# Kernel tuning notes

Measured on AMD Instinct MI355X. Metric: run time of the kernel, lower is better.

The kernel has to match this reference:

```python
import jax, jax.numpy as jnp
import numpy as np

B, H, W, C = 8, 64, 64, 512
G = 32  # num_groups
EPS = 1e-5


def group_norm(x, scale, bias):
    b, h, w, c = x.shape
    xg = x.reshape(b, h, w, G, c // G)
    mean = jnp.mean(xg, axis=(1, 2, 4), keepdims=True)
    var = jnp.var(xg, axis=(1, 2, 4), keepdims=True)
    xg = (xg - mean) / jnp.sqrt(var + EPS)
    x = xg.reshape(b, h, w, c)
    return x * scale + bias


def conv1x1(x, w, b):
    # NHWC 1x1 conv == channel matmul
    return jnp.einsum('bhwc,cd->bhwd', x, w) + b


def setup_inputs() -> dict:
    key = jax.random.key(0)
    ks = jax.random.split(key, 10)
    init = lambda k, shape: jax.random.normal(k, shape, dtype=jnp.float32) * (1.0 / np.sqrt(C))
    return {
        'x': jax.random.normal(ks[0], (B, H, W, C), dtype=jnp.float32),
        'gn_scale': jnp.ones((C,), dtype=jnp.float32),
        'gn_bias': jnp.zeros((C,), dtype=jnp.float32),
        'wq': init(ks[1], (C, C)), 'bq': jnp.zeros((C,), jnp.float32),
        'wk': init(ks[2], (C, C)), 'bk': jnp.zeros((C,), jnp.float32),
        'wv': init(ks[3], (C, C)), 'bv': jnp.zeros((C,), jnp.float32),
        'wo': init(ks[4], (C, C)), 'bo': jnp.zeros((C,), jnp.float32),
    }


def reference(x, gn_scale, gn_bias, wq, bq, wk, bk, wv, bv, wo, bo):
    h = group_norm(x, gn_scale, gn_bias)
    q = conv1x1(h, wq, bq)
    k = conv1x1(h, wk, bk)
    v = conv1x1(h, wv, bv)
    b, hh, ww, c = h.shape
    n = hh * ww
    q = q.reshape(b, n, c)
    k = k.reshape(b, n, c)
    v = v.reshape(b, n, c)
    scores = jnp.einsum('bqc,bkc->bqk', q, k) * (c ** -0.5)
    attn = jax.nn.softmax(scores, axis=-1)
    out = jnp.einsum('bqk,bkc->bqc', attn, v).reshape(b, hh, ww, c)
    out = conv1x1(out, wo, bo)
    return out + x
```

## Files before the change

kernel.cpp:

```cpp
#include <hip/hip_runtime.h>

typedef __bf16 bfx8 __attribute__((ext_vector_type(8)));
typedef __bf16 bfx4 __attribute__((ext_vector_type(4)));
typedef float  f32x4 __attribute__((ext_vector_type(4)));

#define MFMA16(a,b,c) __builtin_amdgcn_mfma_f32_16x16x32_bf16((a),(b),(c),0,0,0)

static constexpr int BATCH = 8;
static constexpr int NTOK  = 4096;
static constexpr int CH    = 512;
static constexpr float GN_EPS = 1e-5f;
static constexpr float ATT_SCALE = 0.044194173824159216f;

__device__ __forceinline__ void gload16(const void* g, void* l)
{
    __builtin_amdgcn_global_load_lds(
        (const __attribute__((address_space(1))) unsigned int*)g,
        (__attribute__((address_space(3))) unsigned int*)l, 16, 0, 0);
}

__global__ __launch_bounds__(256)
void prep_weights(const float* __restrict__ wq, const float* __restrict__ wk,
                  const float* __restrict__ wv, const float* __restrict__ wo,
                  const float* __restrict__ bq, const float* __restrict__ bk,
                  const float* __restrict__ bv,
                  __bf16* __restrict__ wqkvT, __bf16* __restrict__ woT,
                  float* __restrict__ bqkv)
{
    __shared__ __bf16 t[32][36];
    const int z  = blockIdx.z;
    const float* src = (z == 0) ? wq : (z == 1) ? wk : (z == 2) ? wv : wo;
    const int c0 = blockIdx.x * 32, n0 = blockIdx.y * 32;
    const int tid = threadIdx.x;
    const int r = tid >> 3, c4 = (tid & 7) * 4;

    f32x4 in = *(const f32x4*)&src[(size_t)(c0 + r) * 512 + n0 + c4];
    bfx4 tv;
#pragma unroll
    for (int i = 0; i < 4; ++i) tv[i] = (__bf16)in[i];
    *(bfx4*)&t[r][c4] = tv;
    __syncthreads();
    bfx4 o;
#pragma unroll
    for (int i = 0; i < 4; ++i) o[i] = t[c4 + i][r];
    if (z < 3)
        *(bfx4*)&wqkvT[((size_t)(z * 512 + n0 + r)) * 512 + c0 + c4] = o;
    else
        *(bfx4*)&woT[((size_t)(n0 + r)) * 512 + c0 + c4] = o;

    if (z < 3 && blockIdx.x == 0 && blockIdx.y == 0) {
        const float* bs = (z == 0) ? bq : (z == 1) ? bk : bv;
        bqkv[z * 512 + tid]       = bs[tid];
        bqkv[z * 512 + tid + 256] = bs[tid + 256];
    }
}

__global__ __launch_bounds__(256)
void gn_stats(const float* __restrict__ x, const float* __restrict__ gs,
              const float* __restrict__ gb,
              float* __restrict__ scA, float* __restrict__ biA)
{
    const int g = blockIdx.x, b = blockIdx.y;
    const int tid = threadIdx.x;
    const int half = tid & 1;
    const size_t base = (size_t)b * NTOK * CH + g * 16 + half * 8;

    float sum = 0.f, sumsq = 0.f;
    for (int i = tid; i < 2 * NTOK; i += 256) {
        const int s = i >> 1;
        f32x4 v0 = *(const f32x4*)&x[base + (size_t)s * CH];
        f32x4 v1 = *(const f32x4*)&x[base + (size_t)s * CH + 4];
#pragma unroll
        for (int j = 0; j < 4; ++j) {
            sum += v0[j] + v1[j];
            sumsq += v0[j] * v0[j] + v1[j] * v1[j];
        }
    }
#pragma unroll
    for (int o = 32; o; o >>= 1) { sum += __shfl_down(sum, o); sumsq += __shfl_down(sumsq, o); }
    __shared__ float red[8];
    __shared__ float stats[2];
    const int w = tid >> 6;
    if ((tid & 63) == 0) { red[w] = sum; red[4 + w] = sumsq; }
    __syncthreads();
    if (tid == 0) {
        float s1 = red[0] + red[1] + red[2] + red[3];
        float s2 = red[4] + red[5] + red[6] + red[7];
        float mean = s1 * (1.f / 65536.f);
        float var  = s2 * (1.f / 65536.f) - mean * mean;
        stats[0] = mean; stats[1] = rsqrtf(var + GN_EPS);
    }
    __syncthreads();
    if (tid < 16) {
        const int ch = g * 16 + tid;
        const float sc = gs[ch] * stats[1];
        scA[b * 512 + ch] = sc;
        biA[b * 512 + ch] = gb[ch] - stats[0] * sc;
    }
}

__global__ __launch_bounds__(256)
void gemm_qkv(const float* __restrict__ x, const float* __restrict__ scA,
              const float* __restrict__ biA, const __bf16* __restrict__ Bt,
              const float* __restrict__ bias,
              __bf16* __restrict__ qk, __bf16* __restrict__ vT)
{
    const int bm = blockIdx.x * 128, bn = blockIdx.y * 128;
    const int tid = threadIdx.x;
    const int w = tid >> 6, lane = tid & 63, quad = lane >> 4, l15 = lane & 15;
    const int wm = (w >> 1) * 64, wn = (w & 1) * 64;
    const int brow = bm >> 12;

    __shared__ __attribute__((aligned(16))) __bf16 smem_g[5120 + 2 * 128 * 32];
    __bf16 (*As)[40] = (__bf16(*)[40])smem_g;
    __bf16 (*Bs)[128][32] = (__bf16(*)[128][32])(smem_g + 5120);

    f32x4 acc[4][4];
#pragma unroll
    for (int i = 0; i < 4; ++i)
#pragma unroll
        for (int j = 0; j < 4; ++j) acc[i][j] = (f32x4){0.f, 0.f, 0.f, 0.f};

    const int sr = tid >> 2, scol = (tid & 3) * 8;
    const int brow_l = (lane >> 2);
    const int bcp    = lane & 3;

#pragma unroll
    for (int u = 0; u < 2; ++u) {
        const int row = w * 32 + u * 16 + brow_l;
        gload16(Bt + (size_t)(bn + row) * 512 + ((bcp ^ (row & 3)) * 8),
                &Bs[0][w * 32 + u * 16][0]);
    }
    f32x4 xa0 = *(const f32x4*)&x[(size_t)(bm + sr) * 512 + scol];
    f32x4 xa1 = *(const f32x4*)&x[(size_t)(bm + sr) * 512 + scol + 4];
    f32x4 xb0 = *(const f32x4*)&x[(size_t)(bm + sr + 64) * 512 + scol];
    f32x4 xb1 = *(const f32x4*)&x[(size_t)(bm + sr + 64) * 512 + scol + 4];

    for (int k0 = 0; k0 < 512; k0 += 32) {
        const int cur = (k0 >> 5) & 1;
        __syncthreads();
        {
            const float* scp = scA + brow * 512 + k0 + scol;
            const float* bip = biA + brow * 512 + k0 + scol;
            f32x4 s0v = *(const f32x4*)&scp[0], s1v = *(const f32x4*)&scp[4];
            f32x4 b0v = *(const f32x4*)&bip[0], b1v = *(const f32x4*)&bip[4];
            bfx8 ha, hb;
#pragma unroll
            for (int j = 0; j < 4; ++j) {
                ha[j]     = (__bf16)(xa0[j] * s0v[j] + b0v[j]);
                ha[4 + j] = (__bf16)(xa1[j] * s1v[j] + b1v[j]);
                hb[j]     = (__bf16)(xb0[j] * s0v[j] + b0v[j]);
                hb[4 + j] = (__bf16)(xb1[j] * s1v[j] + b1v[j]);
            }
            *(bfx8*)&As[sr][scol]      = ha;
            *(bfx8*)&As[sr + 64][scol] = hb;
        }
        if (k0 + 32 < 512) {
            const int k1 = k0 + 32;
#pragma unroll
            for (int u = 0; u < 2; ++u) {
                const int row = w * 32 + u * 16 + brow_l;
                gload16(Bt + (size_t)(bn + row) * 512 + k1 + ((bcp ^ (row & 3)) * 8),
                        &Bs[cur ^ 1][w * 32 + u * 16][0]);
            }
            xa0 = *(const f32x4*)&x[(size_t)(bm + sr) * 512 + k1 + scol];
            xa1 = *(const f32x4*)&x[(size_t)(bm + sr) * 512 + k1 + scol + 4];
            xb0 = *(const f32x4*)&x[(size_t)(bm + sr + 64) * 512 + k1 + scol];
            xb1 = *(const f32x4*)&x[(size_t)(bm + sr + 64) * 512 + k1 + scol + 4];
        }
        asm volatile("s_waitcnt lgkmcnt(0)\n\ts_barrier" ::: "memory");

        bfx8 af[4], bfr[4];
#pragma unroll
        for (int mi = 0; mi < 4; ++mi) af[mi] = *(const bfx8*)&As[wm + mi * 16 + l15][quad * 8];
#pragma unroll
        for (int ni = 0; ni < 4; ++ni) {
            const int row = wn + ni * 16 + l15;
            bfr[ni] = *(const bfx8*)&Bs[cur][row][(quad ^ (row & 3)) * 8];
        }
#pragma unroll
        for (int mi = 0; mi < 4; ++mi)
#pragma unroll
            for (int ni = 0; ni < 4; ++ni)
                acc[mi][ni] = MFMA16(af[mi], bfr[ni], acc[mi][ni]);
    }

    if (blockIdx.y < 8) {
        const float scale = (blockIdx.y < 4) ? ATT_SCALE : 1.0f;
#pragma unroll
        for (int ni = 0; ni < 4; ++ni) {
            const int col = bn + wn + ni * 16 + l15;
            const float bv = bias[col];
#pragma unroll
            for (int mi = 0; mi < 4; ++mi)
#pragma unroll
                for (int rr = 0; rr < 4; ++rr) {
                    const int row = bm + wm + mi * 16 + quad * 4 + rr;
                    qk[(size_t)row * 1024 + col] = (__bf16)((acc[mi][ni][rr] + bv) * scale);
                }
        }
    } else {
        const int vch0 = bn - 1024;
        const int tokbase = bm & 4095;
        __bf16* tb = smem_g;
        __syncthreads();
#pragma unroll
        for (int chunk = 0; chunk < 2; ++chunk) {
            if ((w & 1) == chunk) {
#pragma unroll
                for (int ni = 0; ni < 4; ++ni) {
                    const int chc = ni * 16 + l15;
                    const float bv = bias[bn + chunk * 64 + chc];
#pragma unroll
                    for (int mi = 0; mi < 4; ++mi)
#pragma unroll
                        for (int rr = 0; rr < 4; ++rr) {
                            const int tok = wm + mi * 16 + quad * 4 + rr;
                            tb[chc * 136 + tok] = (__bf16)(acc[mi][ni][rr] + bv);
                        }
                }
            }
            __syncthreads();
            {
                const int chn = tid >> 2, t0 = (tid & 3) * 32;
                const size_t gb0 =
                    ((size_t)(brow * 512 + vch0 + chunk * 64 + chn)) * 4096 + tokbase;
#pragma unroll
                for (int u = 0; u < 4; ++u)
                    *(bfx8*)&vT[gb0 + t0 + u * 8] = *(const bfx8*)&tb[chn * 136 + t0 + u * 8];
            }
            __syncthreads();
        }
    }
}

__global__ __launch_bounds__(512, 2)
void attn_fused(const __bf16* __restrict__ qk, const __bf16* __restrict__ vT,
                const __bf16* __restrict__ woT, const float* __restrict__ bo,
                const float* __restrict__ x, float* __restrict__ out)
{
    const int lin = blockIdx.x + (int)gridDim.x * blockIdx.y;
    const int swz = (lin & 7) * 32 + (lin >> 3);
    const int bb  = swz >> 5;
    const int q0  = (swz & 31) * 128;
    const int tid = threadIdx.x;
    const int w = tid >> 6, lane = tid & 63, quad = lane >> 4, l15 = lane & 15;

    __shared__ __attribute__((aligned(16))) unsigned char smem[141312];
    __bf16 (*Ks)[32][512]      = (__bf16(*)[32][512])smem;
    __bf16 (*Vs)[32][4][16][8] = (__bf16(*)[32][4][16][8])(smem + 65536);
    __bf16 (*Ph)[40]           = (__bf16(*)[40])(smem + 131072);
    __bf16 (*Obuf)[520]        = (__bf16(*)[520])smem;

    bfx8 qf[16];
    {
        const __bf16* qptr = qk + ((size_t)(bb * NTOK + q0 + w * 16 + l15)) * 1024;
#pragma unroll
        for (int kk = 0; kk < 16; ++kk)
            qf[kk] = *(const bfx8*)&qptr[kk * 32 + quad * 8];
    }

    f32x4 oacc[32];
#pragma unroll
    for (int i = 0; i < 32; ++i) oacc[i] = (f32x4){0.f, 0.f, 0.f, 0.f};
    float mcur = -1e30f, lcur = 0.f;

#pragma unroll
    for (int u = 0; u < 4; ++u) {
        const int r = w * 4 + u;
        gload16(qk + ((size_t)(bb * NTOK + r)) * 1024 + 512 + ((lane ^ (r & 7)) * 8),
                &Ks[0][r][0]);
    }
#pragma unroll
    for (int u = 0; u < 4; ++u) {
        const int g = w * 4 + u;
        gload16(vT + ((size_t)(bb * 512 + g * 16 + (lane & 15))) * 4096 + (lane >> 4) * 8,
                &Vs[0][g][0][0][0]);
    }

    const int NT = NTOK / 32;
    int buf = 0;
    for (int kt = 0; kt < NT; ++kt) {
        __syncthreads();

        if (kt + 1 < NT) {
            const int kv1 = (kt + 1) * 32;
            const int nb = buf ^ 1;
#pragma unroll
            for (int u = 0; u < 4; ++u) {
                const int r = w * 4 + u;
                gload16(qk + ((size_t)(bb * NTOK + kv1 + r)) * 1024 + 512 + ((lane ^ (r & 7)) * 8),
                        &Ks[nb][r][0]);
            }
#pragma unroll
            for (int u = 0; u < 4; ++u) {
                const int g = w * 4 + u;
                gload16(vT + ((size_t)(bb * 512 + g * 16 + (lane & 15))) * 4096 + kv1 + (lane >> 4) * 8,
                        &Vs[nb][g][0][0][0]);
            }
        }

        f32x4 s0 = (f32x4){0.f, 0.f, 0.f, 0.f}, s1 = (f32x4){0.f, 0.f, 0.f, 0.f};
        __builtin_amdgcn_s_setprio(1);
#pragma unroll
        for (int kk = 0; kk < 16; ++kk) {
            const int pc = (((kk * 4 + quad) ^ (l15 & 7)) * 8);
            bfx8 kb0 = *(const bfx8*)&Ks[buf][l15][pc];
            bfx8 kb1 = *(const bfx8*)&Ks[buf][16 + l15][pc];
            s0 = MFMA16(kb0, qf[kk], s0);
            s1 = MFMA16(kb1, qf[kk], s1);
        }
        __builtin_amdgcn_s_setprio(0);

        float mx = -1e30f;
#pragma unroll
        for (int i = 0; i < 4; ++i) mx = fmaxf(mx, fmaxf(s0[i], s1[i]));
        float ps = 0.f;
        bfx4 pl0, pl1;
#pragma unroll
        for (int i = 0; i < 4; ++i) { float p = __expf(s0[i] - mcur); ps += p; pl0[i] = (__bf16)p; }
#pragma unroll
        for (int i = 0; i < 4; ++i) { float p = __expf(s1[i] - mcur); ps += p; pl1[i] = (__bf16)p; }
        mx = fmaxf(mx, __shfl_xor(mx, 16));
        mx = fmaxf(mx, __shfl_xor(mx, 32));
        if (__builtin_expect(__any(mx > mcur + 8.f), 0)) {
            const float mnew = fmaxf(mcur, mx);
            const float al = __expf(mcur - mnew);
            lcur *= al;
            ps = 0.f;
#pragma unroll
            for (int i = 0; i < 4; ++i) { float p = __expf(s0[i] - mnew); ps += p; pl0[i] = (__bf16)p; }
#pragma unroll
            for (int i = 0; i < 4; ++i) { float p = __expf(s1[i] - mnew); ps += p; pl1[i] = (__bf16)p; }
            mcur = mnew;
#pragma unroll
            for (int ct = 0; ct < 32; ++ct)
#pragma unroll
                for (int r = 0; r < 4; ++r) oacc[ct][r] *= al;
        }

        *(bfx4*)&Ph[w * 16 + l15][quad * 4]      = pl0;
        *(bfx4*)&Ph[w * 16 + l15][16 + quad * 4] = pl1;

        asm volatile("s_waitcnt lgkmcnt(0)" ::: "memory");
        bfx8 pa = *(const bfx8*)&Ph[w * 16 + l15][quad * 8];

        __builtin_amdgcn_s_setprio(1);
#pragma unroll
        for (int ct = 0; ct < 32; ++ct) {
            bfx8 vb = *(const bfx8*)&Vs[buf][ct][quad][l15][0];
            oacc[ct] = MFMA16(vb, pa, oacc[ct]);
        }
        __builtin_amdgcn_s_setprio(0);

        ps += __shfl_xor(ps, 16);
        ps += __shfl_xor(ps, 32);
        lcur += ps;
        buf ^= 1;
    }

#pragma unroll
    for (int h = 0; h < 2; ++h) {
        __syncthreads();
        if ((w >> 2) == h) {
            const float linv = 1.f / lcur;
#pragma unroll
            for (int ct = 0; ct < 32; ++ct) {
                bfx4 ov;
#pragma unroll
                for (int r = 0; r < 4; ++r) ov[r] = (__bf16)(oacc[ct][r] * linv);
                *(bfx4*)&Obuf[(w & 3) * 16 + l15][ct * 16 + quad * 4] = ov;
            }
        }
        __syncthreads();

        const int rs  = (w & 3) * 16;
        const int nt0 = (w >> 2) * 16;
        bfx8 af2[16];
#pragma unroll
        for (int k0 = 0; k0 < 16; ++k0)
            af2[k0] = *(const bfx8*)&Obuf[rs + l15][k0 * 32 + quad * 8];
#pragma unroll 4
        for (int nt = 0; nt < 16; ++nt) {
            f32x4 a2 = (f32x4){0.f, 0.f, 0.f, 0.f};
#pragma unroll
            for (int k0 = 0; k0 < 16; ++k0) {
                bfx8 wb = *(const bfx8*)&woT[(size_t)((nt0 + nt) * 16 + l15) * 512 + k0 * 32 + quad * 8];
                a2 = MFMA16(af2[k0], wb, a2);
            }
            const int col = (nt0 + nt) * 16 + l15;
            const float bv = bo[col];
#pragma unroll
            for (int rr = 0; rr < 4; ++rr) {
                const size_t idx =
                    ((size_t)(bb * NTOK + q0 + h * 64 + rs + quad * 4 + rr)) * 512 + col;
                out[idx] = a2[rr] + bv + x[idx];
            }
        }
    }
}

extern "C" void kernel_launch(void* const* d_in, const int* in_sizes, int n_in,
                              void* d_out, int out_size, void* d_ws, size_t ws_size,
                              hipStream_t stream)
{
    const float* x  = (const float*)d_in[0];
    const float* gs = (const float*)d_in[1];
    const float* gb = (const float*)d_in[2];
    const float* wq = (const float*)d_in[3];
    const float* bq = (const float*)d_in[4];
    const float* wk = (const float*)d_in[5];
    const float* bk = (const float*)d_in[6];
    const float* wv = (const float*)d_in[7];
    const float* bv = (const float*)d_in[8];
    const float* wo = (const float*)d_in[9];
    const float* bo = (const float*)d_in[10];
    float* out = (float*)d_out;

    char* ws = (char*)d_ws;
    __bf16* qk    = (__bf16*)(ws);
    __bf16* vT    = (__bf16*)(ws + 67108864);
    __bf16* wqkvT = (__bf16*)(ws + 100663296);
    __bf16* woT   = (__bf16*)(ws + 102236160);
    float*  bqkv  = (float* )(ws + 102760448);
    float*  scA   = (float* )(ws + 102766592);
    float*  biA   = (float* )(ws + 102782976);

    prep_weights<<<dim3(16, 16, 4), 256, 0, stream>>>(wq, wk, wv, wo, bq, bk, bv,
                                                      wqkvT, woT, bqkv);
    gn_stats<<<dim3(32, BATCH), 256, 0, stream>>>(x, gs, gb, scA, biA);
    gemm_qkv<<<dim3(256, 12), 256, 0, stream>>>(x, scA, biA, wqkvT, bqkv, qk, vT);
    attn_fused<<<dim3(NTOK / 128, BATCH), 512, 0, stream>>>(qk, vT, woT, bo, x, out);
}
```

Measured before the change: 714.3 us.

## Store Q/K in FP8 and compute attention scores with FP8 MFMA

The QKV GEMM now writes Q and K as FP8 (e4m3) bytes instead of bf16, and the attention kernel computes QK^T with the fp8 16x16x32 MFMA, applying the softmax scale afterwards. This halves Q/K storage and the K tile traffic into LDS, shrinking shared memory per block. It also removes the last-iteration branch on prefetch by wrapping the tile index, and preloads the first four V fragments before the softmax to hide LDS latency. The trade-off is reduced precision in the attention scores, which may hurt accuracy.

```diff
diff --git a/kernel.cpp b/kernel.cpp
--- a/kernel.cpp
+++ b/kernel.cpp
@@ -5,6 +5,7 @@
 typedef float  f32x4 __attribute__((ext_vector_type(4)));
 
 #define MFMA16(a,b,c) __builtin_amdgcn_mfma_f32_16x16x32_bf16((a),(b),(c),0,0,0)
+#define MFMA16F8(a,b,c) __builtin_amdgcn_mfma_f32_16x16x32_fp8_fp8((a),(b),(c),0,0,0)
 
 static constexpr int BATCH = 8;
 static constexpr int NTOK  = 4096;
@@ -17,6 +18,11 @@
     __builtin_amdgcn_global_load_lds(
         (const __attribute__((address_space(1))) unsigned int*)g,
         (__attribute__((address_space(3))) unsigned int*)l, 16, 0, 0);
+}
+
+__device__ __forceinline__ int cvt2fp8(float a, float b)
+{
+    return __builtin_amdgcn_cvt_pk_fp8_f32(a, b, 0, false);
 }
 
 __global__ __launch_bounds__(256)
@@ -103,7 +109,7 @@
 void gemm_qkv(const float* __restrict__ x, const float* __restrict__ scA,
               const float* __restrict__ biA, const __bf16* __restrict__ Bt,
               const float* __restrict__ bias,
-              __bf16* __restrict__ qk, __bf16* __restrict__ vT)
+              unsigned char* __restrict__ qk8, __bf16* __restrict__ vT)
 {
     const int bm = blockIdx.x * 128, bn = blockIdx.y * 128;
     const int tid = threadIdx.x;
@@ -186,18 +192,20 @@
     }
 
     if (blockIdx.y < 8) {
-        const float scale = (blockIdx.y < 4) ? ATT_SCALE : 1.0f;
 #pragma unroll
         for (int ni = 0; ni < 4; ++ni) {
             const int col = bn + wn + ni * 16 + l15;
             const float bv = bias[col];
 #pragma unroll
-            for (int mi = 0; mi < 4; ++mi)
-#pragma unroll
-                for (int rr = 0; rr < 4; ++rr) {
-                    const int row = bm + wm + mi * 16 + quad * 4 + rr;
-                    qk[(size_t)row * 1024 + col] = (__bf16)((acc[mi][ni][rr] + bv) * scale);
-                }
+            for (int mi = 0; mi < 4; ++mi) {
+                const int row0 = bm + wm + mi * 16 + quad * 4;
+                const int p01 = cvt2fp8(acc[mi][ni][0] + bv, acc[mi][ni][1] + bv);
+                const int p23 = cvt2fp8(acc[mi][ni][2] + bv, acc[mi][ni][3] + bv);
+                qk8[(size_t)(row0 + 0) * 1024 + col] = (unsigned char)(p01 & 0xff);
+                qk8[(size_t)(row0 + 1) * 1024 + col] = (unsigned char)((p01 >> 8) & 0xff);
+                qk8[(size_t)(row0 + 2) * 1024 + col] = (unsigned char)(p23 & 0xff);
+                qk8[(size_t)(row0 + 3) * 1024 + col] = (unsigned char)((p23 >> 8) & 0xff);
+            }
         }
     } else {
         const int vch0 = bn - 1024;
@@ -235,7 +243,7 @@
 }
 
 __global__ __launch_bounds__(512, 2)
-void attn_fused(const __bf16* __restrict__ qk, const __bf16* __restrict__ vT,
+void attn_fused(const unsigned char* __restrict__ qk8, const __bf16* __restrict__ vT,
                 const __bf16* __restrict__ woT, const float* __restrict__ bo,
                 const float* __restrict__ x, float* __restrict__ out)
 {
@@ -246,18 +254,18 @@
     const int tid = threadIdx.x;
     const int w = tid >> 6, lane = tid & 63, quad = lane >> 4, l15 = lane & 15;
 
-    __shared__ __attribute__((aligned(16))) unsigned char smem[141312];
-    __bf16 (*Ks)[32][512]      = (__bf16(*)[32][512])smem;
-    __bf16 (*Vs)[32][4][16][8] = (__bf16(*)[32][4][16][8])(smem + 65536);
-    __bf16 (*Ph)[40]           = (__bf16(*)[40])(smem + 131072);
-    __bf16 (*Obuf)[520]        = (__bf16(*)[520])smem;
-
-    bfx8 qf[16];
+    __shared__ __attribute__((aligned(16))) unsigned char smem[108544];
+    unsigned char (*Ks8)[32][512] = (unsigned char(*)[32][512])smem;
+    __bf16 (*Vs)[32][4][16][8]    = (__bf16(*)[32][4][16][8])(smem + 32768);
+    __bf16 (*Ph)[40]              = (__bf16(*)[40])(smem + 98304);
+    __bf16 (*Obuf)[520]           = (__bf16(*)[520])smem;
+
+    long qf8[16];
     {
-        const __bf16* qptr = qk + ((size_t)(bb * NTOK + q0 + w * 16 + l15)) * 1024;
+        const unsigned char* qptr = qk8 + ((size_t)(bb * NTOK + q0 + w * 16 + l15)) * 1024;
 #pragma unroll
         for (int kk = 0; kk < 16; ++kk)
-            qf[kk] = *(const bfx8*)&qptr[kk * 32 + quad * 8];
+            qf8[kk] = *(const long*)(qptr + kk * 32 + quad * 8);
     }
 
     f32x4 oacc[32];
@@ -266,15 +274,16 @@
     float mcur = -1e30f, lcur = 0.f;
 
 #pragma unroll
-    for (int u = 0; u < 4; ++u) {
-        const int r = w * 4 + u;
-        gload16(qk + ((size_t)(bb * NTOK + r)) * 1024 + 512 + ((lane ^ (r & 7)) * 8),
-                &Ks[0][r][0]);
+    for (int u = 0; u < 2; ++u) {
+        const int r = w * 4 + u * 2 + (lane >> 5);
+        const int srcoff = ((2 * (lane & 31)) ^ ((r & 7) << 1)) * 8;
+        gload16(qk8 + ((size_t)(bb * NTOK + r)) * 1024 + 512 + srcoff,
+                &Ks8[0][w * 4 + u * 2][0]);
     }
 #pragma unroll
     for (int u = 0; u < 4; ++u) {
         const int g = w * 4 + u;
-        gload16(vT + ((size_t)(bb * 512 + g * 16 + (lane & 15))) * 4096 + (lane >> 4) * 8,
+        gload16(vT + ((size_t)(bb * 512 + g * 16 + l15)) * 4096 + quad * 8,
                 &Vs[0][g][0][0][0]);
     }
 
@@ -283,19 +292,20 @@
     for (int kt = 0; kt < NT; ++kt) {
         __syncthreads();
 
-        if (kt + 1 < NT) {
-            const int kv1 = (kt + 1) * 32;
+        {
+            const int kv1 = ((kt + 1) & (NT - 1)) * 32;
             const int nb = buf ^ 1;
 #pragma unroll
-            for (int u = 0; u < 4; ++u) {
-                const int r = w * 4 + u;
-                gload16(qk + ((size_t)(bb * NTOK + kv1 + r)) * 1024 + 512 + ((lane ^ (r & 7)) * 8),
-                        &Ks[nb][r][0]);
+            for (int u = 0; u < 2; ++u) {
+                const int r = w * 4 + u * 2 + (lane >> 5);
+                const int srcoff = ((2 * (lane & 31)) ^ ((r & 7) << 1)) * 8;
+                gload16(qk8 + ((size_t)(bb * NTOK + kv1 + r)) * 1024 + 512 + srcoff,
+                        &Ks8[nb][w * 4 + u * 2][0]);
             }
 #pragma unroll
             for (int u = 0; u < 4; ++u) {
                 const int g = w * 4 + u;
-                gload16(vT + ((size_t)(bb * 512 + g * 16 + (lane & 15))) * 4096 + kv1 + (lane >> 4) * 8,
+                gload16(vT + ((size_t)(bb * 512 + g * 16 + l15)) * 4096 + kv1 + quad * 8,
                         &Vs[nb][g][0][0][0]);
             }
         }
@@ -304,17 +314,25 @@
         __builtin_amdgcn_s_setprio(1);
 #pragma unroll
         for (int kk = 0; kk < 16; ++kk) {
-            const int pc = (((kk * 4 + quad) ^ (l15 & 7)) * 8);
-            bfx8 kb0 = *(const bfx8*)&Ks[buf][l15][pc];
-            bfx8 kb1 = *(const bfx8*)&Ks[buf][16 + l15][pc];
-            s0 = MFMA16(kb0, qf[kk], s0);
-            s1 = MFMA16(kb1, qf[kk], s1);
+            const int pc = (((kk * 4 + quad) ^ ((l15 & 7) << 1)) * 8);
+            long kb0 = *(const long*)&Ks8[buf][l15][pc];
+            long kb1 = *(const long*)&Ks8[buf][16 + l15][pc];
+            s0 = MFMA16F8(kb0, qf8[kk], s0);
+            s1 = MFMA16F8(kb1, qf8[kk], s1);
         }
         __builtin_amdgcn_s_setprio(0);
 
+        bfx8 vpre[4];
+#pragma unroll
+        for (int ct = 0; ct < 4; ++ct)
+            vpre[ct] = *(const bfx8*)&Vs[buf][ct][quad][l15][0];
+
         float mx = -1e30f;
 #pragma unroll
-        for (int i = 0; i < 4; ++i) mx = fmaxf(mx, fmaxf(s0[i], s1[i]));
+        for (int i = 0; i < 4; ++i) {
+            s0[i] *= ATT_SCALE; s1[i] *= ATT_SCALE;
+            mx = fmaxf(mx, fmaxf(s0[i], s1[i]));
+        }
         float ps = 0.f;
         bfx4 pl0, pl1;
 #pragma unroll
@@ -347,7 +365,10 @@
 
         __builtin_amdgcn_s_setprio(1);
 #pragma unroll
-        for (int ct = 0; ct < 32; ++ct) {
+        for (int ct = 0; ct < 4; ++ct)
+            oacc[ct] = MFMA16(vpre[ct], pa, oacc[ct]);
+#pragma unroll
+        for (int ct = 4; ct < 32; ++ct) {
             bfx8 vb = *(const bfx8*)&Vs[buf][ct][quad][l15][0];
             oacc[ct] = MFMA16(vb, pa, oacc[ct]);
         }
@@ -418,17 +439,17 @@
     float* out = (float*)d_out;
 
     char* ws = (char*)d_ws;
-    __bf16* qk    = (__bf16*)(ws);
-    __bf16* vT    = (__bf16*)(ws + 67108864);
-    __bf16* wqkvT = (__bf16*)(ws + 100663296);
-    __bf16* woT   = (__bf16*)(ws + 102236160);
-    float*  bqkv  = (float* )(ws + 102760448);
-    float*  scA   = (float* )(ws + 102766592);
-    float*  biA   = (float* )(ws + 102782976);
+    unsigned char* qk8 = (unsigned char*)(ws);
+    __bf16* vT    = (__bf16*)(ws + 33554432);
+    __bf16* wqkvT = (__bf16*)(ws + 67108864);
+    __bf16* woT   = (__bf16*)(ws + 68681728);
+    float*  bqkv  = (float* )(ws + 69206016);
+    float*  scA   = (float* )(ws + 69212160);
+    float*  biA   = (float* )(ws + 69228544);
 
     prep_weights<<<dim3(16, 16, 4), 256, 0, stream>>>(wq, wk, wv, wo, bq, bk, bv,
                                                       wqkvT, woT, bqkv);
     gn_stats<<<dim3(32, BATCH), 256, 0, stream>>>(x, gs, gb, scA, biA);
-    gemm_qkv<<<dim3(256, 12), 256, 0, stream>>>(x, scA, biA, wqkvT, bqkv, qk, vT);
-    attn_fused<<<dim3(NTOK / 128, BATCH), 512, 0, stream>>>(qk, vT, woT, bo, x, out);
-}
+    gemm_qkv<<<dim3(256, 12), 256, 0, stream>>>(x, scA, biA, wqkvT, bqkv, qk8, vT);
+    attn_fused<<<dim3(NTOK / 128, BATCH), 512, 0, stream>>>(qk8, vT, woT, bo, x, out);
+}
```

After: 918.3 us. 1.29x slower.
